# Performance work log

Hardware: AMD Instinct MI355X
Metric: run time of the kernel (lower is better)

## Reference

```python
import jax, jax.numpy as jnp
import numpy as np
from jax import lax

BIG = jnp.float32(1e10)  # initial 'infinite' min-distance


def farthest_point_sampling(points, nsamples):
    """Exact iterative FPS. points: (B, P, 3) -> indices (B, nsamples) int32.

    The KD-tree partitioning in QuickFPS is an acceleration structure; the
    reference math is the canonical running-min-distance / argmax FPS.
    """
    B, P, _ = points.shape

    def step(carry, _):
        min_d, last_idx = carry
        # (B, 1, 3) coordinates of the most recently selected point
        last_pt = jnp.take_along_axis(points, last_idx[:, None, None], axis=1)
        d = jnp.sum((points - last_pt) ** 2, axis=-1)  # (B, P)
        min_d = jnp.minimum(min_d, d)
        nxt = jnp.argmax(min_d, axis=-1).astype(jnp.int32)  # (B,)
        return (min_d, nxt), nxt

    init_idx = jnp.zeros((B,), jnp.int32)  # CUDA FPS starts from point 0
    init_d = jnp.full((B, P), BIG, dtype=points.dtype)
    (_, _), rest = lax.scan(step, (init_d, init_idx), None, length=nsamples - 1)
    # rest: (nsamples-1, B) -> (B, nsamples)
    indices = jnp.concatenate([init_idx[None, :], rest], axis=0).T
    return indices


def setup_inputs() -> dict:
    key = jax.random.key(0)
    points = jax.random.normal(key, (32, 65536, 3), dtype=jnp.float32)
    return {"points": points}


def reference(points):
    nsamples = 1024
    indices = farthest_point_sampling(points, nsamples)  # (B, nsamples)
    # gather_points: (B, nsamples, 3)
    sampled_points = jnp.take_along_axis(points, indices[:, :, None], axis=1)
    return indices, sampled_points
```

## Files before the change

### kernel.cpp

```cpp
#include <hip/hip_runtime.h>

#define NB 32
#define NP 65536
#define NS 1024
#define NT 1024
#define BPB 8
#define CHUNK (NP / BPB)
#define PPT (CHUNK / NT)

typedef unsigned long long u64;
typedef unsigned int u32;
typedef int int4v __attribute__((ext_vector_type(4)));
typedef float f2 __attribute__((ext_vector_type(2)));

__global__ __launch_bounds__(NT) void fps_v15(const float* __restrict__ pts,
                                              float* __restrict__ out,
                                              u32* __restrict__ slots) {
#pragma clang fp contract(off)
    const int bid = blockIdx.x;
    const int b = bid >> 3;
    const int j = bid & 7;
    const int t = threadIdx.x;
    const int wave = t >> 6;
    const int lane = t & 63;
    const int base = j * CHUNK;
    const float* __restrict__ pb = pts + (size_t)b * NP * 3;
    float* __restrict__ out_idx = out + (size_t)b * NS;
    float* __restrict__ out_pts = out + (size_t)NB * NS + (size_t)b * NS * 3;
    u32* __restrict__ slot_b = slots + (size_t)b * NS * BPB * 8;

    __shared__ float P[CHUNK * 3];
    __shared__ u64 cand[NT / 64];
    __shared__ int sel_hist[NS];
    __shared__ float qsh[3];

    {
        const float4* __restrict__ src4 = (const float4*)(pb + (size_t)base * 3);
        float4* dst4 = (float4*)P;
#pragma unroll
        for (int k = 0; k < (CHUNK * 3 / 4) / NT; ++k) dst4[t + k * NT] = src4[t + k * NT];
    }
    if (t == 0) {
        sel_hist[0] = 0;
        if (j == 0) out_idx[0] = 0.0f;
        qsh[0] = pb[0]; qsh[1] = pb[1]; qsh[2] = pb[2];
    }
    __syncthreads();

    f2 PX[PPT / 2], PY[PPT / 2], PZ[PPT / 2], MD[PPT / 2];
#pragma unroll
    for (int i = 0; i < PPT / 2; ++i) {
        const int li = t * PPT + 2 * i;
        PX[i].x = P[li * 3 + 0];  PX[i].y = P[li * 3 + 3];
        PY[i].x = P[li * 3 + 1];  PY[i].y = P[li * 3 + 4];
        PZ[i].x = P[li * 3 + 2];  PZ[i].y = P[li * 3 + 5];
        MD[i] = (f2){1e10f, 1e10f};
    }
    float qx = qsh[0], qy = qsh[1], qz = qsh[2];

    for (int s = 1; s < NS; ++s) {
        const f2 q2x = {qx, qx}, q2y = {qy, qy}, q2z = {qz, qz};
        float nmv[PPT];
#pragma unroll
        for (int i = 0; i < PPT / 2; ++i) {
            f2 dx = PX[i] - q2x;
            f2 dy = PY[i] - q2y;
            f2 dz = PZ[i] - q2z;
            f2 d = (dx * dx + dy * dy) + dz * dz;
            f2 nm;
            nm.x = fminf(MD[i].x, d.x);
            nm.y = fminf(MD[i].y, d.y);
            MD[i] = nm;
            nmv[2 * i] = nm.x;
            nmv[2 * i + 1] = nm.y;
        }
        float bv = fmaxf(fmaxf(fmaxf(nmv[0], nmv[1]), fmaxf(nmv[2], nmv[3])),
                         fmaxf(fmaxf(nmv[4], nmv[5]), fmaxf(nmv[6], nmv[7])));
        float m = bv;
#pragma unroll
        for (int d1 = 32; d1 >= 1; d1 >>= 1) m = fmaxf(m, __shfl_xor(m, d1, 64));
        u64 msk = __ballot(bv == m);
        int src = __ffsll((unsigned long long)msk) - 1;
        int kk = PPT - 1;
#pragma unroll
        for (int k2 = PPT - 2; k2 >= 0; --k2) kk = (nmv[k2] == bv) ? k2 : kk;
        int biw = __shfl(t * PPT + kk, src, 64);
        if (lane == 0)
            cand[wave] = ((u64)__float_as_uint(m) << 32) |
                         (u64)(0xFFFFFFFFu - (u32)(base + biw));
        __syncthreads();
        if (wave == 0) {
            u64 c = cand[lane & 15];
#pragma unroll
            for (int d1 = 8; d1 >= 1; d1 >>= 1) {
                u64 o = __shfl_xor(c, d1, 64);
                c = (o > c) ? o : c;
            }
            const int g0 = (int)(0xFFFFFFFFu - (u32)(c & 0xFFFFFFFFull));
            float wx0 = 0.f, wy0 = 0.f, wz0 = 0.f;
            if (lane == 0) {
                const int lw = g0 - base;
                wx0 = P[lw * 3 + 0];
                wy0 = P[lw * 3 + 1];
                wz0 = P[lw * 3 + 2];
                int4v h0, h1;
                h0.x = (int)(u32)(c & 0xFFFFFFFFull);
                h0.y = (int)(u32)(c >> 32);
                h0.z = __float_as_int(wx0);
                h0.w = __float_as_int(wy0);
                h1.x = h0.x;
                h1.y = h0.y;
                h1.z = __float_as_int(wz0);
                h1.w = 0;
                u32* sp = slot_b + ((size_t)s * BPB + j) * 8;
                asm volatile(
                    "global_store_dwordx4 %0, %2, off sc0 sc1\n\t"
                    "global_store_dwordx4 %1, %3, off sc0 sc1"
                    :: "v"(sp), "v"(sp + 4), "v"(h0), "v"(h1) : "memory");
            }
            if (lane < BPB) {
                u64 k = c;
                float wx = 0.f, wy = 0.f, wz = 0.f;
                if (lane != j) {
                    const u32* sp = slot_b + ((size_t)s * BPB + lane) * 8;
                    int4v a, bb;
                    for (;;) {
                        asm volatile(
                            "global_load_dwordx4 %0, %2, off sc0 sc1\n\t"
                            "global_load_dwordx4 %1, %3, off sc0 sc1\n\t"
                            "s_waitcnt vmcnt(0)"
                            : "=&v"(a), "=&v"(bb)
                            : "v"(sp), "v"(sp + 4) : "memory");
                        if (a.x != 0 && a.x == bb.x && a.y == bb.y) break;
                    }
                    k = ((u64)(u32)a.y << 32) | (u32)a.x;
                    wx = __int_as_float(a.z);
                    wy = __int_as_float(a.w);
                    wz = __int_as_float(bb.z);
                }
#pragma unroll
                for (int d1 = 4; d1 >= 1; d1 >>= 1) {
                    u64 o = __shfl_xor(k, d1, 64);
                    k = (o > k) ? o : k;
                }
                const int g = (int)(0xFFFFFFFFu - (u32)(k & 0xFFFFFFFFull));
                const int jw = (g >> 13) & 7;
                float sx = __shfl(wx, jw, 64);
                float sy = __shfl(wy, jw, 64);
                float sz = __shfl(wz, jw, 64);
                if (lane == 0) {
                    sel_hist[s] = g;
                    if (jw == j) { qsh[0] = wx0; qsh[1] = wy0; qsh[2] = wz0; }
                    else         { qsh[0] = sx;  qsh[1] = sy;  qsh[2] = sz;  }
                    if (j == 0) out_idx[s] = (float)g;
                }
            }
        }
        __syncthreads();
        qx = qsh[0]; qy = qsh[1]; qz = qsh[2];
    }

    if (j == 0) {
        const int gi = sel_hist[t];
        const float* __restrict__ p = pb + (size_t)gi * 3;
        out_pts[(size_t)t * 3 + 0] = p[0];
        out_pts[(size_t)t * 3 + 1] = p[1];
        out_pts[(size_t)t * 3 + 2] = p[2];
    }
}

__global__ __launch_bounds__(NT) void fps_single(const float* __restrict__ pts,
                                                 float* __restrict__ out) {
#pragma clang fp contract(off)
    const int b = blockIdx.x;
    const int t = threadIdx.x;
    const float* __restrict__ pb = pts + (size_t)b * NP * 3;
    float* __restrict__ out_idx = out + (size_t)b * NS;
    float* __restrict__ out_pts = out + (size_t)NB * NS + (size_t)b * NS * 3;
    __shared__ int sel_hist[NS];
    __shared__ u64 cand[16];
    __shared__ int sel_sh;
    float md[NP / NT];
#pragma unroll
    for (int i = 0; i < NP / NT; ++i) md[i] = 1e10f;
    if (t == 0) { sel_hist[0] = 0; out_idx[0] = 0.0f; }
    float qx = pb[0], qy = pb[1], qz = pb[2];
    const int wave = t >> 6;
    const int lane = t & 63;
    for (int s = 1; s < NS; ++s) {
        float bestv = -1.0f;
        int besti = 0;
#pragma unroll
        for (int i = 0; i < NP / NT; ++i) {
            const int gi = t + i * NT;
            const float* __restrict__ p = pb + (size_t)gi * 3;
            float dx = p[0] - qx, dy = p[1] - qy, dz = p[2] - qz;
            float d = (dx * dx + dy * dy) + dz * dz;
            float nmd = fminf(md[i], d);
            md[i] = nmd;
            if (nmd > bestv) { bestv = nmd; besti = gi; }
        }
        u64 pk = ((u64)__float_as_uint(bestv) << 32) |
                 (u64)(0xFFFFFFFFu - (u32)besti);
#pragma unroll
        for (int m = 32; m >= 1; m >>= 1) {
            u64 o = __shfl_xor(pk, m, 64);
            pk = (o > pk) ? o : pk;
        }
        if (lane == 0) cand[wave] = pk;
        __syncthreads();
        if (wave == 0) {
            u64 c = (lane < 16) ? cand[lane] : 0ull;
#pragma unroll
            for (int m = 8; m >= 1; m >>= 1) {
                u64 o = __shfl_xor(c, m, 64);
                c = (o > c) ? o : c;
            }
            if (lane == 0) {
                int w = (int)(0xFFFFFFFFu - (u32)(c & 0xFFFFFFFFull));
                sel_sh = w; sel_hist[s] = w; out_idx[s] = (float)w;
            }
        }
        __syncthreads();
        const int sel = sel_sh;
        qx = pb[(size_t)sel * 3]; qy = pb[(size_t)sel * 3 + 1]; qz = pb[(size_t)sel * 3 + 2];
    }
    __syncthreads();
    {
        const int gi = sel_hist[t];
        const float* __restrict__ p = pb + (size_t)gi * 3;
        out_pts[(size_t)t * 3 + 0] = p[0];
        out_pts[(size_t)t * 3 + 1] = p[1];
        out_pts[(size_t)t * 3 + 2] = p[2];
    }
}

extern "C" void kernel_launch(void* const* d_in, const int* in_sizes, int n_in,
                              void* d_out, int out_size, void* d_ws, size_t ws_size,
                              hipStream_t stream) {
    const float* pts = (const float*)d_in[0];
    float* out = (float*)d_out;
    (void)in_sizes; (void)n_in; (void)out_size;

    const size_t v15_bytes = (size_t)NB * NS * BPB * 32;
    if (ws_size >= v15_bytes) {
        u32* slots = (u32*)d_ws;
        hipMemsetAsync(d_ws, 0, v15_bytes, stream);
        void* args[] = {(void*)&pts, (void*)&out, (void*)&slots};
        hipLaunchCooperativeKernel((const void*)fps_v15, dim3(NB * BPB), dim3(NT),
                                   args, 0, stream);
    } else {
        hipLaunchKernelGGL(fps_single, dim3(NB), dim3(NT), 0, stream, pts, out);
    }
}
```

Baseline: 2.135 ms.

## Replace second block barrier with LDS flag spin and double-buffered candidates

Removes the second __syncthreads per FPS step. Wave 0 now publishes the next query point through shared memory plus a step tag, and the other waves spin on that tag with s_sleep. The per-wave candidate array is double-buffered by step parity so the next step's writes cannot overwrite values wave 0 is still reading. Wave 0 also keeps the query point in registers, broadcast across the wave, instead of rereading it from shared memory. The cost is busy-waiting waves issuing LDS polls, and correctness now depends on fence ordering within the block.

```diff
diff --git a/kernel.cpp b/kernel.cpp
--- a/kernel.cpp
+++ b/kernel.cpp
@@ -13,7 +13,7 @@
 typedef int int4v __attribute__((ext_vector_type(4)));
 typedef float f2 __attribute__((ext_vector_type(2)));
 
-__global__ __launch_bounds__(NT) void fps_v15(const float* __restrict__ pts,
+__global__ __launch_bounds__(NT) void fps_v16(const float* __restrict__ pts,
                                               float* __restrict__ out,
                                               u32* __restrict__ slots) {
 #pragma clang fp contract(off)
@@ -30,9 +30,10 @@
     u32* __restrict__ slot_b = slots + (size_t)b * NS * BPB * 8;
 
     __shared__ float P[CHUNK * 3];
-    __shared__ u64 cand[NT / 64];
+    __shared__ u64 cand[2][NT / 64];
     __shared__ int sel_hist[NS];
     __shared__ float qsh[3];
+    __shared__ int qtag;
 
     {
         const float4* __restrict__ src4 = (const float4*)(pb + (size_t)base * 3);
@@ -42,8 +43,8 @@
     }
     if (t == 0) {
         sel_hist[0] = 0;
+        qtag = 0;
         if (j == 0) out_idx[0] = 0.0f;
-        qsh[0] = pb[0]; qsh[1] = pb[1]; qsh[2] = pb[2];
     }
     __syncthreads();
 
@@ -56,9 +57,10 @@
         PZ[i].x = P[li * 3 + 2];  PZ[i].y = P[li * 3 + 5];
         MD[i] = (f2){1e10f, 1e10f};
     }
-    float qx = qsh[0], qy = qsh[1], qz = qsh[2];
+    float qx = pb[0], qy = pb[1], qz = pb[2];
 
     for (int s = 1; s < NS; ++s) {
+        const int par = s & 1;
         const f2 q2x = {qx, qx}, q2y = {qy, qy}, q2z = {qz, qz};
         float nmv[PPT];
 #pragma unroll
@@ -86,31 +88,26 @@
         for (int k2 = PPT - 2; k2 >= 0; --k2) kk = (nmv[k2] == bv) ? k2 : kk;
         int biw = __shfl(t * PPT + kk, src, 64);
         if (lane == 0)
-            cand[wave] = ((u64)__float_as_uint(m) << 32) |
-                         (u64)(0xFFFFFFFFu - (u32)(base + biw));
+            cand[par][wave] = ((u64)__float_as_uint(m) << 32) |
+                              (u64)(0xFFFFFFFFu - (u32)(base + biw));
         __syncthreads();
         if (wave == 0) {
-            u64 c = cand[lane & 15];
+            u64 c = cand[par][lane & 15];
 #pragma unroll
             for (int d1 = 8; d1 >= 1; d1 >>= 1) {
                 u64 o = __shfl_xor(c, d1, 64);
                 c = (o > c) ? o : c;
             }
-            const int g0 = (int)(0xFFFFFFFFu - (u32)(c & 0xFFFFFFFFull));
-            float wx0 = 0.f, wy0 = 0.f, wz0 = 0.f;
             if (lane == 0) {
-                const int lw = g0 - base;
-                wx0 = P[lw * 3 + 0];
-                wy0 = P[lw * 3 + 1];
-                wz0 = P[lw * 3 + 2];
+                const int lw = (int)(0xFFFFFFFFu - (u32)c) - base;
                 int4v h0, h1;
-                h0.x = (int)(u32)(c & 0xFFFFFFFFull);
+                h0.x = (int)(u32)c;
                 h0.y = (int)(u32)(c >> 32);
-                h0.z = __float_as_int(wx0);
-                h0.w = __float_as_int(wy0);
+                h0.z = __float_as_int(P[lw * 3 + 0]);
+                h0.w = __float_as_int(P[lw * 3 + 1]);
                 h1.x = h0.x;
                 h1.y = h0.y;
-                h1.z = __float_as_int(wz0);
+                h1.z = __float_as_int(P[lw * 3 + 2]);
                 h1.w = 0;
                 u32* sp = slot_b + ((size_t)s * BPB + j) * 8;
                 asm volatile(
@@ -118,48 +115,58 @@
                     "global_store_dwordx4 %1, %3, off sc0 sc1"
                     :: "v"(sp), "v"(sp + 4), "v"(h0), "v"(h1) : "memory");
             }
-            if (lane < BPB) {
-                u64 k = c;
-                float wx = 0.f, wy = 0.f, wz = 0.f;
-                if (lane != j) {
-                    const u32* sp = slot_b + ((size_t)s * BPB + lane) * 8;
-                    int4v a, bb;
-                    for (;;) {
-                        asm volatile(
-                            "global_load_dwordx4 %0, %2, off sc0 sc1\n\t"
-                            "global_load_dwordx4 %1, %3, off sc0 sc1\n\t"
-                            "s_waitcnt vmcnt(0)"
-                            : "=&v"(a), "=&v"(bb)
-                            : "v"(sp), "v"(sp + 4) : "memory");
-                        if (a.x != 0 && a.x == bb.x && a.y == bb.y) break;
-                    }
-                    k = ((u64)(u32)a.y << 32) | (u32)a.x;
-                    wx = __int_as_float(a.z);
-                    wy = __int_as_float(a.w);
-                    wz = __int_as_float(bb.z);
+            u64 k = c;
+            float wx = 0.f, wy = 0.f, wz = 0.f;
+            if (lane < BPB && lane != j) {
+                const u32* sp = slot_b + ((size_t)s * BPB + lane) * 8;
+                int4v a, bb;
+                for (;;) {
+                    asm volatile(
+                        "global_load_dwordx4 %0, %2, off sc0 sc1\n\t"
+                        "global_load_dwordx4 %1, %3, off sc0 sc1\n\t"
+                        "s_waitcnt vmcnt(0)"
+                        : "=&v"(a), "=&v"(bb)
+                        : "v"(sp), "v"(sp + 4) : "memory");
+                    if (a.x != 0 && a.x == bb.x && a.y == bb.y) break;
                 }
-#pragma unroll
-                for (int d1 = 4; d1 >= 1; d1 >>= 1) {
-                    u64 o = __shfl_xor(k, d1, 64);
-                    k = (o > k) ? o : k;
-                }
-                const int g = (int)(0xFFFFFFFFu - (u32)(k & 0xFFFFFFFFull));
-                const int jw = (g >> 13) & 7;
-                float sx = __shfl(wx, jw, 64);
-                float sy = __shfl(wy, jw, 64);
-                float sz = __shfl(wz, jw, 64);
-                if (lane == 0) {
-                    sel_hist[s] = g;
-                    if (jw == j) { qsh[0] = wx0; qsh[1] = wy0; qsh[2] = wz0; }
-                    else         { qsh[0] = sx;  qsh[1] = sy;  qsh[2] = sz;  }
-                    if (j == 0) out_idx[s] = (float)g;
-                }
-            }
-        }
-        __syncthreads();
-        qx = qsh[0]; qy = qsh[1]; qz = qsh[2];
-    }
-
+                k = ((u64)(u32)a.y << 32) | (u32)a.x;
+                wx = __int_as_float(a.z);
+                wy = __int_as_float(a.w);
+                wz = __int_as_float(bb.z);
+            }
+#pragma unroll
+            for (int d1 = 4; d1 >= 1; d1 >>= 1) {
+                u64 o = __shfl_xor(k, d1, 64);
+                k = (o > k) ? o : k;
+            }
+            k = __shfl(k, 0, 64);
+            const int g = (int)(0xFFFFFFFFu - (u32)(k & 0xFFFFFFFFull));
+            const int jw = (g >> 13) & 7;
+            if (jw == j) {
+                const int lw = g - base;
+                qx = P[lw * 3 + 0];
+                qy = P[lw * 3 + 1];
+                qz = P[lw * 3 + 2];
+            } else {
+                qx = __shfl(wx, jw, 64);
+                qy = __shfl(wy, jw, 64);
+                qz = __shfl(wz, jw, 64);
+            }
+            if (lane == 0) {
+                sel_hist[s] = g;
+                if (j == 0) out_idx[s] = (float)g;
+                qsh[0] = qx; qsh[1] = qy; qsh[2] = qz;
+                __threadfence_block();
+                qtag = s;
+            }
+        } else {
+            while (*(volatile int*)&qtag != s) __builtin_amdgcn_s_sleep(1);
+            __threadfence_block();
+            qx = qsh[0]; qy = qsh[1]; qz = qsh[2];
+        }
+    }
+
+    __syncthreads();
     if (j == 0) {
         const int gi = sel_hist[t];
         const float* __restrict__ p = pb + (size_t)gi * 3;
@@ -242,12 +249,12 @@
     float* out = (float*)d_out;
     (void)in_sizes; (void)n_in; (void)out_size;
 
-    const size_t v15_bytes = (size_t)NB * NS * BPB * 32;
-    if (ws_size >= v15_bytes) {
+    const size_t v16_bytes = (size_t)NB * NS * BPB * 32;
+    if (ws_size >= v16_bytes) {
         u32* slots = (u32*)d_ws;
-        hipMemsetAsync(d_ws, 0, v15_bytes, stream);
+        hipMemsetAsync(d_ws, 0, v16_bytes, stream);
         void* args[] = {(void*)&pts, (void*)&out, (void*)&slots};
-        hipLaunchCooperativeKernel((const void*)fps_v15, dim3(NB * BPB), dim3(NT),
+        hipLaunchCooperativeKernel((const void*)fps_v16, dim3(NB * BPB), dim3(NT),
                                    args, 0, stream);
     } else {
         hipLaunchKernelGGL(fps_single, dim3(NB), dim3(NT), 0, stream, pts, out);
```

New measurement: 2.317 ms. 8.5% more time.
